# Kernel tuning notes

Hardware: AMD Instinct MI355X
Metric: run time of the kernel (lower is better)

## Reference

```python
import jax, jax.numpy as jnp
import numpy as np

B, T, D, H = 2, 2048, 1024, 16
HD = D // H

def setup_inputs() -> dict:
    key = jax.random.key(0)
    ks = jax.random.split(key, 5)
    fan = D
    bound_w = float(np.sqrt(6.0 / fan))  # kaiming_uniform-ish scale
    return {
        "x": jax.random.normal(ks[0], (B, T, D), dtype=jnp.float32),
        "W_qkv": jax.random.uniform(ks[1], (3 * D, D), minval=-bound_w, maxval=bound_w, dtype=jnp.float32),
        "b_qkv": jax.random.uniform(ks[2], (3 * D,), minval=-bound_w, maxval=bound_w, dtype=jnp.float32),
        "W_proj": jax.random.uniform(ks[3], (D, D), minval=-bound_w, maxval=bound_w, dtype=jnp.float32),
        "b_proj": jax.random.uniform(ks[4], (D,), minval=-bound_w, maxval=bound_w, dtype=jnp.float32),
    }

def reference(x, W_qkv, b_qkv, W_proj, b_proj):
    Bx, Tx, C = x.shape
    h, hd = H, C // H
    qkv = x @ W_qkv.T + b_qkv                      # (B,T,3C)
    q, k, v = jnp.split(qkv, 3, axis=-1)
    # (B,T,C) -> (B,h,T,hd)
    q = q.reshape(Bx, Tx, h, hd).transpose(0, 2, 1, 3)
    k = k.reshape(Bx, Tx, h, hd).transpose(0, 2, 1, 3)
    v = v.reshape(Bx, Tx, h, hd).transpose(0, 2, 1, 3)
    scale = hd ** -0.5
    scores = jnp.einsum('bhqd,bhkd->bhqk', q, k) * scale
    causal = jnp.tril(jnp.ones((Tx, Tx), dtype=bool))
    scores = jnp.where(causal, scores, -jnp.inf)
    weights = jax.nn.softmax(scores, axis=-1)      # stable softmax, same math
    out = jnp.einsum('bhqk,bhkd->bhqd', weights, v)
    out = out.transpose(0, 2, 1, 3).reshape(Bx, Tx, C)
    return out @ W_proj.T + b_proj
```

## Files before the change

kernel.cpp:

```cpp
#include <hip/hip_runtime.h>

typedef unsigned short u16;
typedef __attribute__((ext_vector_type(8))) short bf16x8;
typedef __attribute__((ext_vector_type(4))) float f32x4;

#define Bb 2
#define Tt 2048
#define Dd 1024
#define Hh 16
#define HD 64
#define NTOK (Bb*Tt)
#define QKVN (3*Dd)

__device__ __forceinline__ u16 f2b(float f) {
    unsigned u = __float_as_uint(f);
    unsigned r = (u + 0x7fffu + ((u >> 16) & 1u)) >> 16;
    return (u16)r;
}

__device__ __forceinline__ void g2l16(const u16* g, u16* l) {
    __builtin_amdgcn_global_load_lds(
        (const __attribute__((address_space(1))) unsigned int*)g,
        (__attribute__((address_space(3))) unsigned int*)l,
        16, 0, 0);
}

__device__ __forceinline__ unsigned pk2(float lo, float hi) {
    return __builtin_amdgcn_perm(__float_as_uint(hi), __float_as_uint(lo), 0x07060302u);
}

#define N4X  (NTOK * Dd / 4)
#define N4WQ (3 * Dd * Dd / 4)
#define N4WP (Dd * Dd / 4)
__global__ void cvt_all(const float* __restrict__ x, const float* __restrict__ wq,
                        const float* __restrict__ wp, u16* __restrict__ xb,
                        u16* __restrict__ wqb, u16* __restrict__ wpb) {
    int i = blockIdx.x * blockDim.x + threadIdx.x;
    const float* src; u16* dst; int j;
    if (i < N4X)                { src = x;  dst = xb;  j = i; }
    else if (i < N4X + N4WQ)    { src = wq; dst = wqb; j = i - N4X; }
    else                        { src = wp; dst = wpb; j = i - N4X - N4WQ; }
    float4 f = ((const float4*)src)[j];
    ushort4 o;
    o.x = f2b(f.x); o.y = f2b(f.y); o.z = f2b(f.z); o.w = f2b(f.w);
    ((ushort4*)dst)[j] = o;
}

template<int MODE>
__global__ __launch_bounds__(256, 2)
void gemm_bt(const u16* __restrict__ A, const u16* __restrict__ Bt,
             const float* __restrict__ bias, int M, int N, int K,
             u16* __restrict__ C16, float* __restrict__ Co) {
    __shared__ alignas(16) u16 As[128 * 32];
    __shared__ alignas(16) u16 Bs[128 * 32];
    const int tid = threadIdx.x;
    const int wave = tid >> 6, lane = tid & 63;
    const int quad = lane >> 4, l16 = lane & 15;
    const int wm = (wave & 1) * 64, wn = (wave >> 1) * 64;
    const int m0 = blockIdx.x * 128, n0 = blockIdx.y * 128;
    const int lrow = lane >> 2, lcol = (lane & 3) << 3;

    f32x4 acc[4][4];
#pragma unroll
    for (int i = 0; i < 4; ++i)
#pragma unroll
        for (int j = 0; j < 4; ++j)
            acc[i][j] = (f32x4){0.f, 0.f, 0.f, 0.f};

    for (int k0 = 0; k0 < K; k0 += 32) {
#pragma unroll
        for (int c = 0; c < 2; ++c) {
            const int rb = (c * 4 + wave) * 16;
            g2l16(A  + (size_t)(m0 + rb + lrow) * K + k0 + lcol, &As[rb * 32 + (lane << 3)]);
            g2l16(Bt + (size_t)(n0 + rb + lrow) * K + k0 + lcol, &Bs[rb * 32 + (lane << 3)]);
        }
        __syncthreads();
        bf16x8 a[4], b[4];
#pragma unroll
        for (int i = 0; i < 4; ++i)
            a[i] = *(const bf16x8*)(&As[(wm + i * 16 + l16) * 32 + quad * 8]);
#pragma unroll
        for (int i = 0; i < 4; ++i)
            b[i] = *(const bf16x8*)(&Bs[(wn + i * 16 + l16) * 32 + quad * 8]);
#pragma unroll
        for (int i = 0; i < 4; ++i)
#pragma unroll
            for (int j = 0; j < 4; ++j)
                acc[i][j] = __builtin_amdgcn_mfma_f32_16x16x32_bf16(a[i], b[j], acc[i][j], 0, 0, 0);
        __syncthreads();
    }

    float b4[4];
#pragma unroll
    for (int j = 0; j < 4; ++j) b4[j] = bias[n0 + wn + j * 16 + l16];

#pragma unroll
    for (int i = 0; i < 4; ++i) {
#pragma unroll
        for (int j = 0; j < 4; ++j) {
#pragma unroll
            for (int r = 0; r < 4; ++r) {
                int m = m0 + wm + i * 16 + quad * 4 + r;
                int n = n0 + wn + j * 16 + l16;
                float v = acc[i][j][r] + b4[j];
                if (MODE == 0) C16[(size_t)m * N + n] = f2b(v);
                else           Co[(size_t)m * N + n] = v;
            }
        }
    }
}

__global__ __launch_bounds__(256)
void transpose_v(const u16* __restrict__ qkv, u16* __restrict__ Vt) {
    __shared__ u16 Ls[64 * 66];
    const int t0 = blockIdx.x * 64, bh = blockIdx.y;
    const int hh = bh & (Hh - 1), bidx = bh >> 4;
    const int tid = threadIdx.x;
    const int r = tid >> 2, c = (tid & 3) << 4;
    const u16* src = qkv + (size_t)(bidx * Tt + t0 + r) * QKVN + 2 * Dd + hh * HD + c;
    *(uint4*)(&Ls[r * 66 + c]) = *(const uint4*)src;
    *(uint4*)(&Ls[r * 66 + c + 8]) = *(const uint4*)(src + 8);
    __syncthreads();
    const int d = tid >> 2, tc = (tid & 3) << 4;
    u16 tmp[16];
#pragma unroll
    for (int j = 0; j < 16; ++j) tmp[j] = Ls[(tc + j) * 66 + d];
    u16* dst = Vt + ((size_t)bh * HD + d) * Tt + t0 + tc;
    *(uint4*)(dst)     = *(const uint4*)(tmp);
    *(uint4*)(dst + 8) = *(const uint4*)(tmp + 8);
}

#define LKP 80
#define PSP 84
#define FMX 24.0f

__global__ __launch_bounds__(256, 4)
void attn_fwd(const u16* __restrict__ qkv, const u16* __restrict__ Vt,
              u16* __restrict__ Ao) {
    const int qt = 31 - (int)blockIdx.x;
    const int bh = blockIdx.y;
    const int hh = bh & (Hh - 1), bidx = bh >> 4;
    const u16* Qp = qkv + (size_t)bidx * Tt * QKVN + hh * HD;
    const u16* Kp = Qp + Dd;
    const u16* Vp = Vt + (size_t)bh * HD * Tt;
    const int tid = threadIdx.x;
    const int wave = tid >> 6, lane = tid & 63;
    const int quad = lane >> 4, l16 = lane & 15;

    __shared__ alignas(16) u16 Ks[64 * LKP];
    __shared__ alignas(16) u16 Vs[64 * LKP];
    __shared__ alignas(16) u16 Ps[4][16 * PSP];
    u16* Pw = &Ps[wave][0];

    const int srow = tid >> 3, scol = (tid & 7) << 3;
    const float sc = 0.125f * 1.44269504f;

    const int q0 = qt * 64;
    const int qrow_g = q0 + wave * 16 + l16;
    bf16x8 aq[2];
#pragma unroll
    for (int kk = 0; kk < 2; ++kk)
        aq[kk] = *(const bf16x8*)(Qp + (size_t)qrow_g * QKVN + kk * 32 + quad * 8);

    f32x4 o[4];
#pragma unroll
    for (int nt = 0; nt < 4; ++nt) o[nt] = (f32x4){0.f, 0.f, 0.f, 0.f};
    float lsum = 0.f;
    const int nit = qt + 1;

    uint4 kreg0, kreg1, vreg0, vreg1;
    kreg0 = *(const uint4*)(Kp + (size_t)srow * QKVN + scol);
    kreg1 = *(const uint4*)(Kp + (size_t)(srow + 32) * QKVN + scol);
    vreg0 = *(const uint4*)(Vp + (size_t)srow * Tt + scol);
    vreg1 = *(const uint4*)(Vp + (size_t)(srow + 32) * Tt + scol);

    for (int kt = 0; kt < nit; ++kt) {
        const int k0 = kt * 64;
        *(uint4*)(&Ks[srow * LKP + scol]) = kreg0;
        *(uint4*)(&Ks[(srow + 32) * LKP + scol]) = kreg1;
        *(uint4*)(&Vs[srow * LKP + scol]) = vreg0;
        *(uint4*)(&Vs[(srow + 32) * LKP + scol]) = vreg1;
        __syncthreads();
        if (kt + 1 < nit) {
            const int kn = k0 + 64;
            kreg0 = *(const uint4*)(Kp + (size_t)(kn + srow) * QKVN + scol);
            kreg1 = *(const uint4*)(Kp + (size_t)(kn + srow + 32) * QKVN + scol);
            vreg0 = *(const uint4*)(Vp + (size_t)srow * Tt + kn + scol);
            vreg1 = *(const uint4*)(Vp + (size_t)(srow + 32) * Tt + kn + scol);
        }

        f32x4 s[4];
#pragma unroll
        for (int nt = 0; nt < 4; ++nt) {
            f32x4 z = (f32x4){0.f, 0.f, 0.f, 0.f};
#pragma unroll
            for (int kk = 0; kk < 2; ++kk) {
                bf16x8 ak = *(const bf16x8*)(&Ks[(nt * 16 + l16) * LKP + kk * 32 + quad * 8]);
                z = __builtin_amdgcn_mfma_f32_16x16x32_bf16(ak, aq[kk], z, 0, 0, 0);
            }
            s[nt] = z;
        }

        if (kt == qt) {
#pragma unroll
            for (int nt = 0; nt < 4; ++nt)
#pragma unroll
                for (int r = 0; r < 4; ++r) {
                    int key = k0 + nt * 16 + quad * 4 + r;
                    float t = __builtin_fmaf(s[nt][r], sc, -FMX);
                    t = (key <= qrow_g) ? t : -200.0f;
                    float p = exp2f(t);
                    s[nt][r] = p;
                    lsum += p;
                }
        } else {
#pragma unroll
            for (int nt = 0; nt < 4; ++nt)
#pragma unroll
                for (int r = 0; r < 4; ++r) {
                    float p = exp2f(__builtin_fmaf(s[nt][r], sc, -FMX));
                    s[nt][r] = p;
                    lsum += p;
                }
        }

#pragma unroll
        for (int nt = 0; nt < 4; ++nt) {
            uint2 d;
            d.x = pk2(s[nt][0], s[nt][1]);
            d.y = pk2(s[nt][2], s[nt][3]);
            *(uint2*)(&Pw[l16 * PSP + nt * 16 + quad * 4]) = d;
        }

#pragma unroll
        for (int kk = 0; kk < 2; ++kk) {
            bf16x8 bp = *(const bf16x8*)(&Pw[l16 * PSP + kk * 32 + quad * 8]);
#pragma unroll
            for (int nt = 0; nt < 4; ++nt) {
                bf16x8 av = *(const bf16x8*)(&Vs[(nt * 16 + l16) * LKP + kk * 32 + quad * 8]);
                o[nt] = __builtin_amdgcn_mfma_f32_16x16x32_bf16(av, bp, o[nt], 0, 0, 0);
            }
        }
        __syncthreads();
    }

    lsum += __shfl_xor(lsum, 16, 64);
    lsum += __shfl_xor(lsum, 32, 64);
    const float rinv = 1.0f / lsum;
    u16* orow = Ao + ((size_t)bidx * Tt + qrow_g) * Dd + hh * HD;
#pragma unroll
    for (int nt = 0; nt < 4; ++nt) {
        ushort4 p4;
        p4.x = f2b(o[nt][0] * rinv); p4.y = f2b(o[nt][1] * rinv);
        p4.z = f2b(o[nt][2] * rinv); p4.w = f2b(o[nt][3] * rinv);
        *(ushort4*)(orow + nt * 16 + quad * 4) = p4;
    }
}

extern "C" void kernel_launch(void* const* d_in, const int* in_sizes, int n_in,
                              void* d_out, int out_size, void* d_ws, size_t ws_size,
                              hipStream_t stream) {
    const float* x      = (const float*)d_in[0];
    const float* W_qkv  = (const float*)d_in[1];
    const float* b_qkv  = (const float*)d_in[2];
    const float* W_proj = (const float*)d_in[3];
    const float* b_proj = (const float*)d_in[4];
    float* out = (float*)d_out;

    char* ws = (char*)d_ws;
    u16* Wprojb = (u16*)(ws);
    u16* Wqkvb  = (u16*)(ws + (2u << 20));
    u16* xb     = (u16*)(ws + (8u << 20));
    u16* qkvb   = (u16*)(ws + (16u << 20));
    u16* Vtb    = (u16*)(ws + (40u << 20));
    u16* attnb  = (u16*)(ws + (2u << 20));

    cvt_all<<<(N4X + N4WQ + N4WP) / 256, 256, 0, stream>>>(x, W_qkv, W_proj, xb, Wqkvb, Wprojb);

    {
        dim3 grid(NTOK / 128, QKVN / 128);
        gemm_bt<0><<<grid, 256, 0, stream>>>(xb, Wqkvb, b_qkv, NTOK, QKVN, Dd,
                                             qkvb, nullptr);
    }
    {
        dim3 grid(Tt / 64, Bb * Hh);
        transpose_v<<<grid, 256, 0, stream>>>(qkvb, Vtb);
    }
    {
        dim3 grid(32, Bb * Hh);
        attn_fwd<<<grid, 256, 0, stream>>>(qkvb, Vtb, attnb);
    }
    {
        dim3 grid(NTOK / 128, Dd / 128);
        gemm_bt<1><<<grid, 256, 0, stream>>>(attnb, Wprojb, b_proj, NTOK, Dd, Dd,
                                             nullptr, out);
    }
}
```

Before: 216.1 us.

## Fuse V transpose into QKV GEMM, pair attention tiles, double-buffer K/V, narrow proj tiles

The QKV GEMM epilogue now also writes V transposed, which removes the separate transpose kernel launch and its extra pass over memory, at the cost of scattered strided stores. Attention blocks each process a complementary pair of query tiles (long and short) to balance causal work, and K/V shared-memory tiles are double-buffered with one barrier per iteration. The output projection GEMM uses 128x64 tiles to launch more blocks for the smaller N. Attention occupancy hint drops from 4 to 3 blocks per CU, and the grid is halved to 512 blocks.

```diff
diff --git a/kernel.cpp b/kernel.cpp
--- a/kernel.cpp
+++ b/kernel.cpp
@@ -46,11 +46,11 @@
     ((ushort4*)dst)[j] = o;
 }
 
-template<int MODE>
 __global__ __launch_bounds__(256, 2)
-void gemm_bt(const u16* __restrict__ A, const u16* __restrict__ Bt,
-             const float* __restrict__ bias, int M, int N, int K,
-             u16* __restrict__ C16, float* __restrict__ Co) {
+void gemm_qkv(const u16* __restrict__ A, const u16* __restrict__ Bt,
+              const float* __restrict__ bias,
+              u16* __restrict__ C16, u16* __restrict__ Vt) {
+    const int N = QKVN, K = Dd;
     __shared__ alignas(16) u16 As[128 * 32];
     __shared__ alignas(16) u16 Bs[128 * 32];
     const int tid = threadIdx.x;
@@ -93,6 +93,7 @@
     float b4[4];
 #pragma unroll
     for (int j = 0; j < 4; ++j) b4[j] = bias[n0 + wn + j * 16 + l16];
+    const bool isV = (n0 >= 2 * Dd);
 
 #pragma unroll
     for (int i = 0; i < 4; ++i) {
@@ -102,43 +103,84 @@
             for (int r = 0; r < 4; ++r) {
                 int m = m0 + wm + i * 16 + quad * 4 + r;
                 int n = n0 + wn + j * 16 + l16;
-                float v = acc[i][j][r] + b4[j];
-                if (MODE == 0) C16[(size_t)m * N + n] = f2b(v);
-                else           Co[(size_t)m * N + n] = v;
-            }
-        }
-    }
-}
-
-__global__ __launch_bounds__(256)
-void transpose_v(const u16* __restrict__ qkv, u16* __restrict__ Vt) {
-    __shared__ u16 Ls[64 * 66];
-    const int t0 = blockIdx.x * 64, bh = blockIdx.y;
-    const int hh = bh & (Hh - 1), bidx = bh >> 4;
+                u16 bv = f2b(acc[i][j][r] + b4[j]);
+                C16[(size_t)m * N + n] = bv;
+                if (isV) {
+                    int d = n - 2 * Dd, t = m & 2047, bidx = m >> 11;
+                    Vt[((size_t)(bidx * Hh + (d >> 6)) * HD + (d & 63)) * Tt + t] = bv;
+                }
+            }
+        }
+    }
+}
+
+__global__ __launch_bounds__(256, 2)
+void gemm_proj(const u16* __restrict__ A, const u16* __restrict__ Bt,
+               const float* __restrict__ bias, float* __restrict__ Co) {
+    const int N = Dd, K = Dd;
+    __shared__ alignas(16) u16 As[128 * 32];
+    __shared__ alignas(16) u16 Bs[64 * 32];
     const int tid = threadIdx.x;
-    const int r = tid >> 2, c = (tid & 3) << 4;
-    const u16* src = qkv + (size_t)(bidx * Tt + t0 + r) * QKVN + 2 * Dd + hh * HD + c;
-    *(uint4*)(&Ls[r * 66 + c]) = *(const uint4*)src;
-    *(uint4*)(&Ls[r * 66 + c + 8]) = *(const uint4*)(src + 8);
-    __syncthreads();
-    const int d = tid >> 2, tc = (tid & 3) << 4;
-    u16 tmp[16];
-#pragma unroll
-    for (int j = 0; j < 16; ++j) tmp[j] = Ls[(tc + j) * 66 + d];
-    u16* dst = Vt + ((size_t)bh * HD + d) * Tt + t0 + tc;
-    *(uint4*)(dst)     = *(const uint4*)(tmp);
-    *(uint4*)(dst + 8) = *(const uint4*)(tmp + 8);
+    const int wave = tid >> 6, lane = tid & 63;
+    const int quad = lane >> 4, l16 = lane & 15;
+    const int wm = (wave & 1) * 64, wn = (wave >> 1) * 32;
+    const int m0 = blockIdx.x * 128, n0 = blockIdx.y * 64;
+    const int lrow = lane >> 2, lcol = (lane & 3) << 3;
+
+    f32x4 acc[4][2];
+#pragma unroll
+    for (int i = 0; i < 4; ++i)
+#pragma unroll
+        for (int j = 0; j < 2; ++j)
+            acc[i][j] = (f32x4){0.f, 0.f, 0.f, 0.f};
+
+    for (int k0 = 0; k0 < K; k0 += 32) {
+#pragma unroll
+        for (int c = 0; c < 2; ++c) {
+            const int rb = (c * 4 + wave) * 16;
+            g2l16(A + (size_t)(m0 + rb + lrow) * K + k0 + lcol, &As[rb * 32 + (lane << 3)]);
+        }
+        g2l16(Bt + (size_t)(n0 + wave * 16 + lrow) * K + k0 + lcol, &Bs[(wave * 16) * 32 + (lane << 3)]);
+        __syncthreads();
+        bf16x8 a[4], b[2];
+#pragma unroll
+        for (int i = 0; i < 4; ++i)
+            a[i] = *(const bf16x8*)(&As[(wm + i * 16 + l16) * 32 + quad * 8]);
+#pragma unroll
+        for (int j = 0; j < 2; ++j)
+            b[j] = *(const bf16x8*)(&Bs[(wn + j * 16 + l16) * 32 + quad * 8]);
+#pragma unroll
+        for (int i = 0; i < 4; ++i)
+#pragma unroll
+            for (int j = 0; j < 2; ++j)
+                acc[i][j] = __builtin_amdgcn_mfma_f32_16x16x32_bf16(a[i], b[j], acc[i][j], 0, 0, 0);
+        __syncthreads();
+    }
+
+    float b2[2];
+#pragma unroll
+    for (int j = 0; j < 2; ++j) b2[j] = bias[n0 + wn + j * 16 + l16];
+
+#pragma unroll
+    for (int i = 0; i < 4; ++i)
+#pragma unroll
+        for (int j = 0; j < 2; ++j)
+#pragma unroll
+            for (int r = 0; r < 4; ++r) {
+                int m = m0 + wm + i * 16 + quad * 4 + r;
+                int n = n0 + wn + j * 16 + l16;
+                Co[(size_t)m * N + n] = acc[i][j][r] + b2[j];
+            }
 }
 
 #define LKP 80
 #define PSP 84
 #define FMX 24.0f
 
-__global__ __launch_bounds__(256, 4)
+__global__ __launch_bounds__(256, 3)
 void attn_fwd(const u16* __restrict__ qkv, const u16* __restrict__ Vt,
               u16* __restrict__ Ao) {
-    const int qt = 31 - (int)blockIdx.x;
-    const int bh = blockIdx.y;
+    const int pair = blockIdx.x, bh = blockIdx.y;
     const int hh = bh & (Hh - 1), bidx = bh >> 4;
     const u16* Qp = qkv + (size_t)bidx * Tt * QKVN + hh * HD;
     const u16* Kp = Qp + Dd;
@@ -147,113 +189,130 @@
     const int wave = tid >> 6, lane = tid & 63;
     const int quad = lane >> 4, l16 = lane & 15;
 
-    __shared__ alignas(16) u16 Ks[64 * LKP];
-    __shared__ alignas(16) u16 Vs[64 * LKP];
+    __shared__ alignas(16) u16 Ks[2][64 * LKP];
+    __shared__ alignas(16) u16 Vs[2][64 * LKP];
     __shared__ alignas(16) u16 Ps[4][16 * PSP];
     u16* Pw = &Ps[wave][0];
 
     const int srow = tid >> 3, scol = (tid & 7) << 3;
     const float sc = 0.125f * 1.44269504f;
 
-    const int q0 = qt * 64;
-    const int qrow_g = q0 + wave * 16 + l16;
-    bf16x8 aq[2];
-#pragma unroll
-    for (int kk = 0; kk < 2; ++kk)
-        aq[kk] = *(const bf16x8*)(Qp + (size_t)qrow_g * QKVN + kk * 32 + quad * 8);
-
-    f32x4 o[4];
-#pragma unroll
-    for (int nt = 0; nt < 4; ++nt) o[nt] = (f32x4){0.f, 0.f, 0.f, 0.f};
-    float lsum = 0.f;
-    const int nit = qt + 1;
-
-    uint4 kreg0, kreg1, vreg0, vreg1;
-    kreg0 = *(const uint4*)(Kp + (size_t)srow * QKVN + scol);
-    kreg1 = *(const uint4*)(Kp + (size_t)(srow + 32) * QKVN + scol);
-    vreg0 = *(const uint4*)(Vp + (size_t)srow * Tt + scol);
-    vreg1 = *(const uint4*)(Vp + (size_t)(srow + 32) * Tt + scol);
-
-    for (int kt = 0; kt < nit; ++kt) {
-        const int k0 = kt * 64;
-        *(uint4*)(&Ks[srow * LKP + scol]) = kreg0;
-        *(uint4*)(&Ks[(srow + 32) * LKP + scol]) = kreg1;
-        *(uint4*)(&Vs[srow * LKP + scol]) = vreg0;
-        *(uint4*)(&Vs[(srow + 32) * LKP + scol]) = vreg1;
-        __syncthreads();
-        if (kt + 1 < nit) {
-            const int kn = k0 + 64;
-            kreg0 = *(const uint4*)(Kp + (size_t)(kn + srow) * QKVN + scol);
-            kreg1 = *(const uint4*)(Kp + (size_t)(kn + srow + 32) * QKVN + scol);
-            vreg0 = *(const uint4*)(Vp + (size_t)srow * Tt + kn + scol);
-            vreg1 = *(const uint4*)(Vp + (size_t)(srow + 32) * Tt + kn + scol);
-        }
-
-        f32x4 s[4];
+    for (int half = 0; half < 2; ++half) {
+        const int qt = half ? pair : (31 - pair);
+        const int q0 = qt * 64;
+        const int qrow_g = q0 + wave * 16 + l16;
+        bf16x8 aq[2];
+#pragma unroll
+        for (int kk = 0; kk < 2; ++kk)
+            aq[kk] = *(const bf16x8*)(Qp + (size_t)qrow_g * QKVN + kk * 32 + quad * 8);
+
+        f32x4 o[4];
+#pragma unroll
+        for (int nt = 0; nt < 4; ++nt) o[nt] = (f32x4){0.f, 0.f, 0.f, 0.f};
+        float lsum = 0.f;
+        const int nit = qt + 1;
+
+        {
+            uint4 k0r = *(const uint4*)(Kp + (size_t)srow * QKVN + scol);
+            uint4 k1r = *(const uint4*)(Kp + (size_t)(srow + 32) * QKVN + scol);
+            uint4 v0r = *(const uint4*)(Vp + (size_t)srow * Tt + scol);
+            uint4 v1r = *(const uint4*)(Vp + (size_t)(srow + 32) * Tt + scol);
+            *(uint4*)(&Ks[0][srow * LKP + scol]) = k0r;
+            *(uint4*)(&Ks[0][(srow + 32) * LKP + scol]) = k1r;
+            *(uint4*)(&Vs[0][srow * LKP + scol]) = v0r;
+            *(uint4*)(&Vs[0][(srow + 32) * LKP + scol]) = v1r;
+        }
+        __syncthreads();
+
+        for (int kt = 0; kt < nit; ++kt) {
+            const int cur = kt & 1;
+            const u16* Kc = &Ks[cur][0];
+            const u16* Vc = &Vs[cur][0];
+            uint4 k0r, k1r, v0r, v1r;
+            const bool more = (kt + 1 < nit);
+            if (more) {
+                const int kn = (kt + 1) * 64;
+                k0r = *(const uint4*)(Kp + (size_t)(kn + srow) * QKVN + scol);
+                k1r = *(const uint4*)(Kp + (size_t)(kn + srow + 32) * QKVN + scol);
+                v0r = *(const uint4*)(Vp + (size_t)srow * Tt + kn + scol);
+                v1r = *(const uint4*)(Vp + (size_t)(srow + 32) * Tt + kn + scol);
+            }
+
+            f32x4 s[4];
+#pragma unroll
+            for (int nt = 0; nt < 4; ++nt) {
+                f32x4 z = (f32x4){0.f, 0.f, 0.f, 0.f};
+#pragma unroll
+                for (int kk = 0; kk < 2; ++kk) {
+                    bf16x8 ak = *(const bf16x8*)(&Kc[(nt * 16 + l16) * LKP + kk * 32 + quad * 8]);
+                    z = __builtin_amdgcn_mfma_f32_16x16x32_bf16(ak, aq[kk], z, 0, 0, 0);
+                }
+                s[nt] = z;
+            }
+
+            if (kt == qt) {
+                const int k0 = kt * 64;
+#pragma unroll
+                for (int nt = 0; nt < 4; ++nt)
+#pragma unroll
+                    for (int r = 0; r < 4; ++r) {
+                        int key = k0 + nt * 16 + quad * 4 + r;
+                        float t = __builtin_fmaf(s[nt][r], sc, -FMX);
+                        t = (key <= qrow_g) ? t : -200.0f;
+                        float p = exp2f(t);
+                        s[nt][r] = p;
+                        lsum += p;
+                    }
+            } else {
+#pragma unroll
+                for (int nt = 0; nt < 4; ++nt)
+#pragma unroll
+                    for (int r = 0; r < 4; ++r) {
+                        float p = exp2f(__builtin_fmaf(s[nt][r], sc, -FMX));
+                        s[nt][r] = p;
+                        lsum += p;
+                    }
+            }
+
+#pragma unroll
+            for (int nt = 0; nt < 4; ++nt) {
+                uint2 d;
+                d.x = pk2(s[nt][0], s[nt][1]);
+                d.y = pk2(s[nt][2], s[nt][3]);
+                *(uint2*)(&Pw[l16 * PSP + nt * 16 + quad * 4]) = d;
+            }
+
+#pragma unroll
+            for (int kk = 0; kk < 2; ++kk) {
+                bf16x8 bp = *(const bf16x8*)(&Pw[l16 * PSP + kk * 32 + quad * 8]);
+#pragma unroll
+                for (int nt = 0; nt < 4; ++nt) {
+                    bf16x8 av = *(const bf16x8*)(&Vc[(nt * 16 + l16) * LKP + kk * 32 + quad * 8]);
+                    o[nt] = __builtin_amdgcn_mfma_f32_16x16x32_bf16(av, bp, o[nt], 0, 0, 0);
+                }
+            }
+
+            if (more) {
+                const int nxt = cur ^ 1;
+                *(uint4*)(&Ks[nxt][srow * LKP + scol]) = k0r;
+                *(uint4*)(&Ks[nxt][(srow + 32) * LKP + scol]) = k1r;
+                *(uint4*)(&Vs[nxt][srow * LKP + scol]) = v0r;
+                *(uint4*)(&Vs[nxt][(srow + 32) * LKP + scol]) = v1r;
+            }
+            __syncthreads();
+        }
+
+        lsum += __shfl_xor(lsum, 16, 64);
+        lsum += __shfl_xor(lsum, 32, 64);
+        const float rinv = 1.0f / lsum;
+        u16* orow = Ao + ((size_t)bidx * Tt + qrow_g) * Dd + hh * HD;
 #pragma unroll
         for (int nt = 0; nt < 4; ++nt) {
-            f32x4 z = (f32x4){0.f, 0.f, 0.f, 0.f};
-#pragma unroll
-            for (int kk = 0; kk < 2; ++kk) {
-                bf16x8 ak = *(const bf16x8*)(&Ks[(nt * 16 + l16) * LKP + kk * 32 + quad * 8]);
-                z = __builtin_amdgcn_mfma_f32_16x16x32_bf16(ak, aq[kk], z, 0, 0, 0);
-            }
-            s[nt] = z;
-        }
-
-        if (kt == qt) {
-#pragma unroll
-            for (int nt = 0; nt < 4; ++nt)
-#pragma unroll
-                for (int r = 0; r < 4; ++r) {
-                    int key = k0 + nt * 16 + quad * 4 + r;
-                    float t = __builtin_fmaf(s[nt][r], sc, -FMX);
-                    t = (key <= qrow_g) ? t : -200.0f;
-                    float p = exp2f(t);
-                    s[nt][r] = p;
-                    lsum += p;
-                }
-        } else {
-#pragma unroll
-            for (int nt = 0; nt < 4; ++nt)
-#pragma unroll
-                for (int r = 0; r < 4; ++r) {
-                    float p = exp2f(__builtin_fmaf(s[nt][r], sc, -FMX));
-                    s[nt][r] = p;
-                    lsum += p;
-                }
-        }
-
-#pragma unroll
-        for (int nt = 0; nt < 4; ++nt) {
-            uint2 d;
-            d.x = pk2(s[nt][0], s[nt][1]);
-            d.y = pk2(s[nt][2], s[nt][3]);
-            *(uint2*)(&Pw[l16 * PSP + nt * 16 + quad * 4]) = d;
-        }
-
-#pragma unroll
-        for (int kk = 0; kk < 2; ++kk) {
-            bf16x8 bp = *(const bf16x8*)(&Pw[l16 * PSP + kk * 32 + quad * 8]);
-#pragma unroll
-            for (int nt = 0; nt < 4; ++nt) {
-                bf16x8 av = *(const bf16x8*)(&Vs[(nt * 16 + l16) * LKP + kk * 32 + quad * 8]);
-                o[nt] = __builtin_amdgcn_mfma_f32_16x16x32_bf16(av, bp, o[nt], 0, 0, 0);
-            }
-        }
-        __syncthreads();
-    }
-
-    lsum += __shfl_xor(lsum, 16, 64);
-    lsum += __shfl_xor(lsum, 32, 64);
-    const float rinv = 1.0f / lsum;
-    u16* orow = Ao + ((size_t)bidx * Tt + qrow_g) * Dd + hh * HD;
-#pragma unroll
-    for (int nt = 0; nt < 4; ++nt) {
-        ushort4 p4;
-        p4.x = f2b(o[nt][0] * rinv); p4.y = f2b(o[nt][1] * rinv);
-        p4.z = f2b(o[nt][2] * rinv); p4.w = f2b(o[nt][3] * rinv);
-        *(ushort4*)(orow + nt * 16 + quad * 4) = p4;
+            ushort4 p4;
+            p4.x = f2b(o[nt][0] * rinv); p4.y = f2b(o[nt][1] * rinv);
+            p4.z = f2b(o[nt][2] * rinv); p4.w = f2b(o[nt][3] * rinv);
+            *(ushort4*)(orow + nt * 16 + quad * 4) = p4;
+        }
     }
 }
 
@@ -279,20 +338,14 @@
 
     {
         dim3 grid(NTOK / 128, QKVN / 128);
-        gemm_bt<0><<<grid, 256, 0, stream>>>(xb, Wqkvb, b_qkv, NTOK, QKVN, Dd,
-                                             qkvb, nullptr);
+        gemm_qkv<<<grid, 256, 0, stream>>>(xb, Wqkvb, b_qkv, qkvb, Vtb);
     }
     {
-        dim3 grid(Tt / 64, Bb * Hh);
-        transpose_v<<<grid, 256, 0, stream>>>(qkvb, Vtb);
+        dim3 grid(16, Bb * Hh);
+        attn_fwd<<<grid, 256, 0, stream>>>(qkvb, Vtb, attnb);
     }
     {
-        dim3 grid(32, Bb * Hh);
-        attn_fwd<<<grid, 256, 0, stream>>>(qkvb, Vtb, attnb);
-    }
-    {
-        dim3 grid(NTOK / 128, Dd / 128);
-        gemm_bt<1><<<grid, 256, 0, stream>>>(attnb, Wprojb, b_proj, NTOK, Dd, Dd,
-                                             nullptr, out);
-    }
-}
+        dim3 grid(NTOK / 128, Dd / 64);
+        gemm_proj<<<grid, 256, 0, stream>>>(attnb, Wprojb, b_proj, out);
+    }
+}
```

Measured after the change: 192.3 us. 11.0% less time.
